# Performance work log

Measured on AMD Instinct MI355X. Metric: run time of the kernel, lower is better.

The kernel has to match this reference:

```python
import jax, jax.numpy as jnp
import numpy as np

B, S, H, NH = 2, 2048, 1024, 16
HD = H // NH  # 64
BASE = 10000.0


def _rope_tables(seq_len, head_dim):
    inv_freq = 1.0 / (BASE ** (jnp.arange(0, head_dim, 2, dtype=jnp.float32) / head_dim))
    t = jnp.arange(seq_len, dtype=jnp.float32)
    freqs = jnp.outer(t, inv_freq)            # [S, HD/2]
    emb = jnp.concatenate([freqs, freqs], -1)  # [S, HD]
    return jnp.cos(emb), jnp.sin(emb)


def _rotate_half(x):
    x1, x2 = jnp.split(x, 2, axis=-1)
    return jnp.concatenate([-x2, x1], axis=-1)


def setup_inputs() -> dict:
    key = jax.random.key(0)
    ks = jax.random.split(key, 5)
    sc = 1.0 / np.sqrt(H)
    return {
        "hidden_states": jax.random.normal(ks[0], (B, S, H), jnp.float32),
        "Wq": jax.random.normal(ks[1], (H, H), jnp.float32) * sc,
        "Wk": jax.random.normal(ks[2], (H, H), jnp.float32) * sc,
        "Wv": jax.random.normal(ks[3], (H, H), jnp.float32) * sc,
        "Wo": jax.random.normal(ks[4], (H, H), jnp.float32) * sc,
    }


def reference(hidden_states, Wq, Wk, Wv, Wo):
    b, s, h = hidden_states.shape
    # nn.Linear: y = x @ W.T
    q = hidden_states @ Wq.T
    k = hidden_states @ Wk.T
    v = hidden_states @ Wv.T
    # [B, NH, S, HD]
    q = q.reshape(b, s, NH, HD).transpose(0, 2, 1, 3)
    k = k.reshape(b, s, NH, HD).transpose(0, 2, 1, 3)
    v = v.reshape(b, s, NH, HD).transpose(0, 2, 1, 3)
    cos, sin = _rope_tables(s, HD)  # [S, HD], broadcast over B, NH
    q = q * cos + _rotate_half(q) * sin
    k = k * cos + _rotate_half(k) * sin
    scores = jnp.einsum('bhqd,bhkd->bhqk', q, k) / jnp.sqrt(jnp.float32(HD))
    probs = jax.nn.softmax(scores, axis=-1)
    ctx = jnp.einsum('bhqk,bhkd->bhqd', probs, v)
    ctx = ctx.transpose(0, 2, 1, 3).reshape(b, s, h)
    return ctx @ Wo.T
```

## Files before the change

### kernel.cpp

```cpp
#include <hip/hip_runtime.h>
#include <hip/hip_bf16.h>
#include <math.h>

typedef __hip_bfloat16 bf16;
typedef float f32x4 __attribute__((ext_vector_type(4)));
typedef float f32x16 __attribute__((ext_vector_type(16)));
typedef short s16x8 __attribute__((ext_vector_type(8)));

#define NB 2
#define SEQ 2048
#define HID 1024
#define NHEAD 16
#define HD 64
#define BH (NB * NHEAD)
#define MROWS (NB * SEQ)
#define QSCL 0.18033688011111793f

static __device__ __forceinline__ f32x4 mfma16(s16x8 a, s16x8 b, f32x4 c) {
  return __builtin_amdgcn_mfma_f32_16x16x32_bf16(a, b, c, 0, 0, 0);
}
static __device__ __forceinline__ f32x16 mfma32(s16x8 a, s16x8 b, f32x16 c) {
  return __builtin_amdgcn_mfma_f32_32x32x16_bf16(a, b, c, 0, 0, 0);
}

static __device__ __forceinline__ void gload_lds16(const bf16* g, bf16* l) {
  __builtin_amdgcn_global_load_lds((const __attribute__((address_space(1))) void*)g,
                                   (__attribute__((address_space(3))) void*)l, 16, 0, 0);
}

static __device__ __forceinline__ unsigned pack_bf16(float a, float b) {
  __hip_bfloat162 t = __float22bfloat162_rn(float2{a, b});
  return *(unsigned*)&t;
}

__global__ __launch_bounds__(256) void prep_kernel(const float* __restrict__ X,
                                                   const float* __restrict__ wq, const float* __restrict__ wk,
                                                   const float* __restrict__ wv, const float* __restrict__ wo,
                                                   bf16* __restrict__ Xb, bf16* __restrict__ wqkv,
                                                   bf16* __restrict__ wob,
                                                   float* __restrict__ ct, float* __restrict__ st) {
  int bid = blockIdx.x, tid = threadIdx.x;
  if (bid < 8192) {
    const float* src;
    bf16* dst;
    int i;
    if (bid < 4096) {
      src = X; dst = Xb;
      i = (bid * 256 + tid) * 4;
    } else {
      int wsel = (bid - 4096) >> 10;
      src = (wsel == 0) ? wq : (wsel == 1) ? wk : (wsel == 2) ? wv : wo;
      dst = (wsel < 3) ? (wqkv + (size_t)wsel * HID * HID) : wob;
      i = (((bid - 4096) & 1023) * 256 + tid) * 4;
    }
    float4 v = *(const float4*)(src + i);
    bf16 a0 = __float2bfloat16(v.x), a1 = __float2bfloat16(v.y);
    bf16 a2 = __float2bfloat16(v.z), a3 = __float2bfloat16(v.w);
    ushort4 u;
    u.x = *(const unsigned short*)&a0;
    u.y = *(const unsigned short*)&a1;
    u.z = *(const unsigned short*)&a2;
    u.w = *(const unsigned short*)&a3;
    *(ushort4*)(dst + i) = u;
  } else {
    int i = (bid - 8192) * 256 + tid;
    int s = i >> 5, j = i & 31;
    float inv = expf(-(float)(2 * j) * (9.210340371976184f / 64.0f));
    float ang = (float)s * inv;
    float sn, cs;
    sincosf(ang, &sn, &cs);
    ct[i] = cs;
    st[i] = sn;
  }
}

template <int MODE>
__global__ __launch_bounds__(256) void gemm_bt(const bf16* __restrict__ A, const bf16* __restrict__ Bm,
                                               float* __restrict__ C,
                                               bf16* __restrict__ Qb, bf16* __restrict__ Kb,
                                               bf16* __restrict__ Vtg,
                                               const float* __restrict__ ct, const float* __restrict__ st,
                                               int M, int N, int K) {
  __shared__ __align__(16) bf16 As[128][32];
  __shared__ __align__(16) bf16 Bs[128][32];
  const int tid = threadIdx.x, lane = tid & 63, wid = tid >> 6;
  const int wm = wid >> 1, wn = wid & 1;
  const int tm = blockIdx.y * 128, tn = blockIdx.x * 128;
  const int lrow = lane >> 2;
  const int lcol = (lane & 3) * 8;

  f32x4 acc[4][4];
#pragma unroll
  for (int i = 0; i < 4; ++i)
#pragma unroll
    for (int j = 0; j < 4; ++j) acc[i][j] = (f32x4){0.f, 0.f, 0.f, 0.f};

  for (int k0 = 0; k0 < K; k0 += 32) {
    __syncthreads();
    {
      int r0 = wid * 32;
      gload_lds16(A  + (size_t)(tm + r0 +      lrow) * K + k0 + lcol, &As[r0][0]);
      gload_lds16(A  + (size_t)(tm + r0 + 16 + lrow) * K + k0 + lcol, &As[r0 + 16][0]);
      gload_lds16(Bm + (size_t)(tn + r0 +      lrow) * K + k0 + lcol, &Bs[r0][0]);
      gload_lds16(Bm + (size_t)(tn + r0 + 16 + lrow) * K + k0 + lcol, &Bs[r0 + 16][0]);
    }
    __syncthreads();
    s16x8 af[4], bfr[4];
#pragma unroll
    for (int mi = 0; mi < 4; ++mi)
      af[mi] = *(const s16x8*)&As[wm * 64 + mi * 16 + (lane & 15)][(lane >> 4) * 8];
#pragma unroll
    for (int ni = 0; ni < 4; ++ni)
      bfr[ni] = *(const s16x8*)&Bs[wn * 64 + ni * 16 + (lane & 15)][(lane >> 4) * 8];
#pragma unroll
    for (int mi = 0; mi < 4; ++mi)
#pragma unroll
      for (int ni = 0; ni < 4; ++ni)
        acc[mi][ni] = mfma16(af[mi], bfr[ni], acc[mi][ni]);
  }

  if (MODE == 0) {
    const int tblk = tn >> 10;
    if (tblk < 2) {
      const float scl = (tblk == 0) ? QSCL : 1.0f;
#pragma unroll
      for (int mi = 0; mi < 4; ++mi) {
#pragma unroll
        for (int r = 0; r < 4; ++r) {
          int row = tm + wm * 64 + mi * 16 + (lane >> 4) * 4 + r;
          int s = row & (SEQ - 1);
#pragma unroll
          for (int p = 0; p < 2; ++p) {
            int j = p * 16 + (lane & 15);
            float c = ct[s * 32 + j], sn = st[s * 32 + j];
            float x0 = acc[mi][p][r], x1 = acc[mi][p + 2][r];
            acc[mi][p][r]     = (x0 * c - x1 * sn) * scl;
            acc[mi][p + 2][r] = (x1 * c + x0 * sn) * scl;
          }
        }
      }
    }
  }

#pragma unroll
  for (int mi = 0; mi < 4; ++mi) {
#pragma unroll
    for (int ni = 0; ni < 4; ++ni) {
#pragma unroll
      for (int r = 0; r < 4; ++r) {
        int row = tm + wm * 64 + mi * 16 + (lane >> 4) * 4 + r;
        int col = tn + wn * 64 + ni * 16 + (lane & 15);
        float v = acc[mi][ni][r];
        if (MODE == 0) {
          int t = col >> 10, c = col & (HID - 1);
          int h = c >> 6, d = c & 63;
          int b = row >> 11, s = row & (SEQ - 1);
          size_t bh = (size_t)(b * NHEAD + h);
          if (t == 0)      Qb[(bh * SEQ + s) * HD + d]  = __float2bfloat16(v);
          else if (t == 1) Kb[(bh * SEQ + s) * HD + d]  = __float2bfloat16(v);
          else             Vtg[(bh * HD + d) * SEQ + s] = __float2bfloat16(v);
        } else {
          C[(size_t)row * N + col] = v;
        }
      }
    }
  }
}

__global__ __launch_bounds__(256) void attn_kernel(const bf16* __restrict__ Q, const bf16* __restrict__ K,
                                                   const bf16* __restrict__ Vt, bf16* __restrict__ ctx) {
  __shared__ __align__(16) bf16 S[16384];
  bf16* Ks = S;
  bf16* Vs = S + 8192;
  const int tid = threadIdx.x, l = tid & 63, w = tid >> 6;
  const int lq = l & 31, hi = l >> 5;

  const int id = blockIdx.x;
  const int lin = (id & 7) * 64 + (id >> 3);
  const int bh = lin >> 4, qb = lin & 15;

  const bf16* Qp  = Q  + ((size_t)bh * SEQ + qb * 128) * HD;
  const bf16* Kp0 = K  + (size_t)bh * SEQ * HD;
  const bf16* Vp0 = Vt + (size_t)bh * HD * SEQ;

  s16x8 qf[4];
  {
    const bf16* qr = Qp + (w * 32 + lq) * HD + hi * 8;
#pragma unroll
    for (int ks = 0; ks < 4; ++ks) qf[ks] = *(const s16x8*)(qr + ks * 16);
  }

  const int s0 = tid, s1 = tid + 256;
  const int R0 = s0 >> 3, R1 = s1 >> 3;
  const int c0 = ((s0 & 7) ^ (R0 & 7)) * 8;
  const int c1 = ((s1 & 7) ^ (R1 & 7)) * 8;
  const int p0 = (R0 & 51) | ((R0 & 4) << 1) | ((R0 & 8) >> 1);
  const int p1 = (R1 & 51) | ((R1 & 4) << 1) | ((R1 & 8) >> 1);
  const bf16* kS0 = Kp0 + p0 * HD + c0;
  const bf16* kS1 = Kp0 + p1 * HD + c1;
  const bf16* vS0 = Vp0 + (size_t)R0 * SEQ + c0;
  const bf16* vS1 = Vp0 + (size_t)R1 * SEQ + c1;

#define STAGE(t, b)                                        \
  do {                                                     \
    gload_lds16(kS0 + (t) * (64 * HD), Ks + (b) * 4096 + s0 * 8); \
    gload_lds16(kS1 + (t) * (64 * HD), Ks + (b) * 4096 + s1 * 8); \
    gload_lds16(vS0 + (t) * 64,        Vs + (b) * 4096 + s0 * 8); \
    gload_lds16(vS1 + (t) * 64,        Vs + (b) * 4096 + s1 * 8); \
  } while (0)

  STAGE(0, 0);
  __syncthreads();

  float m_run = -INFINITY, lsum = 0.f;
  f32x16 acc0{}, acc1{};

  const int NT = SEQ / 64;
  for (int kvt = 0; kvt < NT; ++kvt) {
    const int cur = kvt & 1;
    if (kvt + 1 < NT) STAGE(kvt + 1, cur ^ 1);
    const bf16* Kc = Ks + cur * 4096;
    const bf16* Vc = Vs + cur * 4096;

    f32x16 sf0{}, sf1{};
    __builtin_amdgcn_s_setprio(1);
#pragma unroll
    for (int ks = 0; ks < 4; ++ks) {
      const int slot = (ks * 2 + hi) ^ (lq & 7);
      sf0 = mfma32(*(const s16x8*)(Kc + lq * 64 + slot * 8),        qf[ks], sf0);
      sf1 = mfma32(*(const s16x8*)(Kc + (32 + lq) * 64 + slot * 8), qf[ks], sf1);
    }
    __builtin_amdgcn_s_setprio(0);

    float pmax = sf0[0];
#pragma unroll
    for (int i = 1; i < 16; ++i) pmax = fmaxf(pmax, sf0[i]);
#pragma unroll
    for (int i = 0; i < 16; ++i) pmax = fmaxf(pmax, sf1[i]);
    pmax = fmaxf(pmax, __shfl_xor(pmax, 32));

    if (__any(pmax > m_run + 8.f)) {
      float mn = fmaxf(m_run, pmax);
      float corr = __builtin_amdgcn_exp2f(m_run - mn);
      m_run = mn;
      lsum *= corr;
#pragma unroll
      for (int r = 0; r < 16; ++r) {
        float cr = __shfl(corr, (r & 3) + 8 * (r >> 2) + 4 * hi);
        acc0[r] *= cr;
        acc1[r] *= cr;
      }
    }

    float ls = 0.f;
#pragma unroll
    for (int i = 0; i < 16; ++i) {
      sf0[i] = __builtin_amdgcn_exp2f(sf0[i] - m_run);
      ls += sf0[i];
    }
#pragma unroll
    for (int i = 0; i < 16; ++i) {
      sf1[i] = __builtin_amdgcn_exp2f(sf1[i] - m_run);
      ls += sf1[i];
    }
    lsum += ls;

    s16x8 pf[4];
#pragma unroll
    for (int kt = 0; kt < 4; ++kt) {
      union { unsigned u[4]; s16x8 v; } cc;
#pragma unroll
      for (int vv = 0; vv < 4; ++vv) {
        if (kt < 2) cc.u[vv] = pack_bf16(sf0[(kt & 1) * 8 + 2 * vv], sf0[(kt & 1) * 8 + 2 * vv + 1]);
        else        cc.u[vv] = pack_bf16(sf1[(kt & 1) * 8 + 2 * vv], sf1[(kt & 1) * 8 + 2 * vv + 1]);
      }
      pf[kt] = cc.v;
    }

    __builtin_amdgcn_s_setprio(1);
#pragma unroll
    for (int kt = 0; kt < 4; ++kt) {
      const int slot = (kt * 2 + hi) ^ (lq & 7);
      acc0 = mfma32(pf[kt], *(const s16x8*)(Vc + lq * 64 + slot * 8),        acc0);
      acc1 = mfma32(pf[kt], *(const s16x8*)(Vc + (32 + lq) * 64 + slot * 8), acc1);
    }
    __builtin_amdgcn_s_setprio(0);
    __syncthreads();
  }
#undef STAGE

  lsum += __shfl_xor(lsum, 32);
  const int b = bh >> 4, h = bh & (NHEAD - 1);
#pragma unroll
  for (int r = 0; r < 16; ++r) {
    int q = (r & 3) + 8 * (r >> 2) + 4 * hi;
    float inv = 1.0f / __shfl(lsum, q);
    size_t base = ((size_t)b * SEQ + qb * 128 + w * 32 + q) * HID + h * HD + lq;
    ctx[base]      = __float2bfloat16(acc0[r] * inv);
    ctx[base + 32] = __float2bfloat16(acc1[r] * inv);
  }
}

extern "C" void kernel_launch(void* const* d_in, const int* in_sizes, int n_in,
                              void* d_out, int out_size, void* d_ws, size_t ws_size,
                              hipStream_t stream) {
  const float* X  = (const float*)d_in[0];
  const float* Wq = (const float*)d_in[1];
  const float* Wk = (const float*)d_in[2];
  const float* Wv = (const float*)d_in[3];
  const float* Wo = (const float*)d_in[4];

  char* p = (char*)d_ws;
  bf16* Xb   = (bf16*)p; p += (size_t)MROWS * HID * 2;
  bf16* Wqkv = (bf16*)p; p += (size_t)3 * HID * HID * 2;
  bf16* Wob  = (bf16*)p; p += (size_t)HID * HID * 2;
  bf16* Qb   = (bf16*)p; p += (size_t)BH * SEQ * HD * 2;
  bf16* Kb   = (bf16*)p; p += (size_t)BH * SEQ * HD * 2;
  bf16* Vtg  = (bf16*)p; p += (size_t)BH * HD * SEQ * 2;
  bf16* Cb   = (bf16*)p; p += (size_t)MROWS * HID * 2;
  float* ct  = (float*)p; p += (size_t)SEQ * 32 * 4;
  float* st  = (float*)p; p += (size_t)SEQ * 32 * 4;

  prep_kernel<<<8448, 256, 0, stream>>>(X, Wq, Wk, Wv, Wo, Xb, Wqkv, Wob, ct, st);

  gemm_bt<0><<<dim3(3 * HID / 128, MROWS / 128), 256, 0, stream>>>(
      Xb, Wqkv, nullptr, Qb, Kb, Vtg, ct, st, MROWS, 3 * HID, HID);

  attn_kernel<<<dim3(512), 256, 0, stream>>>(Qb, Kb, Vtg, Cb);

  gemm_bt<1><<<dim3(HID / 128, MROWS / 128), 256, 0, stream>>>(
      Cb, Wob, (float*)d_out, nullptr, nullptr, nullptr, nullptr, nullptr, MROWS, HID, HID);
}
```

Before: 140.7 us.

## Split attention KV range across two wave groups and merge partial softmax results

The attention kernel now runs 512 threads per block as two groups of four waves. Each group processes half of the KV sequence for the same 128 query rows, with its own double-buffered LDS staging. The partial outputs, running maxima and sums are merged through shared memory at the end. This doubles the waves available to hide latency and halves the serial loop length per block, at the cost of doubled LDS use (64KB per block), an extra merge pass, and lower block-level occupancy.

```diff
diff --git a/kernel.cpp b/kernel.cpp
--- a/kernel.cpp
+++ b/kernel.cpp
@@ -167,13 +167,13 @@
   }
 }
 
-__global__ __launch_bounds__(256) void attn_kernel(const bf16* __restrict__ Q, const bf16* __restrict__ K,
-                                                   const bf16* __restrict__ Vt, bf16* __restrict__ ctx) {
-  __shared__ __align__(16) bf16 S[16384];
-  bf16* Ks = S;
-  bf16* Vs = S + 8192;
+__global__ __launch_bounds__(512, 4) void attn_kernel(const bf16* __restrict__ Q, const bf16* __restrict__ K,
+                                                      const bf16* __restrict__ Vt, bf16* __restrict__ ctx) {
+  __shared__ __align__(16) bf16 S[32768];
   const int tid = threadIdx.x, l = tid & 63, w = tid >> 6;
   const int lq = l & 31, hi = l >> 5;
+  const int grp = w >> 2, wq = w & 3;
+  const int gtid = tid & 255;
 
   const int id = blockIdx.x;
   const int lin = (id & 7) * 64 + (id >> 3);
@@ -183,14 +183,17 @@
   const bf16* Kp0 = K  + (size_t)bh * SEQ * HD;
   const bf16* Vp0 = Vt + (size_t)bh * HD * SEQ;
 
+  bf16* Ksg = S + grp * 16384;
+  bf16* Vsg = S + grp * 16384 + 8192;
+
   s16x8 qf[4];
   {
-    const bf16* qr = Qp + (w * 32 + lq) * HD + hi * 8;
+    const bf16* qr = Qp + (wq * 32 + lq) * HD + hi * 8;
 #pragma unroll
     for (int ks = 0; ks < 4; ++ks) qf[ks] = *(const s16x8*)(qr + ks * 16);
   }
 
-  const int s0 = tid, s1 = tid + 256;
+  const int s0 = gtid, s1 = gtid + 256;
   const int R0 = s0 >> 3, R1 = s1 >> 3;
   const int c0 = ((s0 & 7) ^ (R0 & 7)) * 8;
   const int c1 = ((s1 & 7) ^ (R1 & 7)) * 8;
@@ -201,26 +204,26 @@
   const bf16* vS0 = Vp0 + (size_t)R0 * SEQ + c0;
   const bf16* vS1 = Vp0 + (size_t)R1 * SEQ + c1;
 
-#define STAGE(t, b)                                        \
-  do {                                                     \
-    gload_lds16(kS0 + (t) * (64 * HD), Ks + (b) * 4096 + s0 * 8); \
-    gload_lds16(kS1 + (t) * (64 * HD), Ks + (b) * 4096 + s1 * 8); \
-    gload_lds16(vS0 + (t) * 64,        Vs + (b) * 4096 + s0 * 8); \
-    gload_lds16(vS1 + (t) * 64,        Vs + (b) * 4096 + s1 * 8); \
+#define STAGE(t, b)                                                 \
+  do {                                                              \
+    gload_lds16(kS0 + (size_t)(t) * (64 * HD), Ksg + (b) * 4096 + s0 * 8); \
+    gload_lds16(kS1 + (size_t)(t) * (64 * HD), Ksg + (b) * 4096 + s1 * 8); \
+    gload_lds16(vS0 + (t) * 64,                Vsg + (b) * 4096 + s0 * 8); \
+    gload_lds16(vS1 + (t) * 64,                Vsg + (b) * 4096 + s1 * 8); \
   } while (0)
 
-  STAGE(0, 0);
+  STAGE(grp * 16, 0);
   __syncthreads();
 
   float m_run = -INFINITY, lsum = 0.f;
   f32x16 acc0{}, acc1{};
 
-  const int NT = SEQ / 64;
-  for (int kvt = 0; kvt < NT; ++kvt) {
-    const int cur = kvt & 1;
-    if (kvt + 1 < NT) STAGE(kvt + 1, cur ^ 1);
-    const bf16* Kc = Ks + cur * 4096;
-    const bf16* Vc = Vs + cur * 4096;
+  const int NSTEP = 16;
+  for (int i = 0; i < NSTEP; ++i) {
+    const int cur = i & 1;
+    if (i + 1 < NSTEP) STAGE(grp * 16 + i + 1, cur ^ 1);
+    const bf16* Kc = Ksg + cur * 4096;
+    const bf16* Vc = Vsg + cur * 4096;
 
     f32x16 sf0{}, sf1{};
     __builtin_amdgcn_s_setprio(1);
@@ -234,9 +237,9 @@
 
     float pmax = sf0[0];
 #pragma unroll
-    for (int i = 1; i < 16; ++i) pmax = fmaxf(pmax, sf0[i]);
-#pragma unroll
-    for (int i = 0; i < 16; ++i) pmax = fmaxf(pmax, sf1[i]);
+    for (int i2 = 1; i2 < 16; ++i2) pmax = fmaxf(pmax, sf0[i2]);
+#pragma unroll
+    for (int i2 = 0; i2 < 16; ++i2) pmax = fmaxf(pmax, sf1[i2]);
     pmax = fmaxf(pmax, __shfl_xor(pmax, 32));
 
     if (__any(pmax > m_run + 8.f)) {
@@ -254,14 +257,14 @@
 
     float ls = 0.f;
 #pragma unroll
-    for (int i = 0; i < 16; ++i) {
-      sf0[i] = __builtin_amdgcn_exp2f(sf0[i] - m_run);
-      ls += sf0[i];
-    }
-#pragma unroll
-    for (int i = 0; i < 16; ++i) {
-      sf1[i] = __builtin_amdgcn_exp2f(sf1[i] - m_run);
-      ls += sf1[i];
+    for (int i2 = 0; i2 < 16; ++i2) {
+      sf0[i2] = __builtin_amdgcn_exp2f(sf0[i2] - m_run);
+      ls += sf0[i2];
+    }
+#pragma unroll
+    for (int i2 = 0; i2 < 16; ++i2) {
+      sf1[i2] = __builtin_amdgcn_exp2f(sf1[i2] - m_run);
+      ls += sf1[i2];
     }
     lsum += ls;
 
@@ -290,14 +293,45 @@
 #undef STAGE
 
   lsum += __shfl_xor(lsum, 32);
-  const int b = bh >> 4, h = bh & (NHEAD - 1);
-#pragma unroll
-  for (int r = 0; r < 16; ++r) {
-    int q = (r & 3) + 8 * (r >> 2) + 4 * hi;
-    float inv = 1.0f / __shfl(lsum, q);
-    size_t base = ((size_t)b * SEQ + qb * 128 + w * 32 + q) * HID + h * HD + lq;
-    ctx[base]      = __float2bfloat16(acc0[r] * inv);
-    ctx[base + 32] = __float2bfloat16(acc1[r] * inv);
+
+  float* Op = (float*)(S + 16384);
+  float* Mp = (float*)(S);
+  float* Lp = Mp + 128;
+
+  if (grp == 1) {
+    if (hi == 0) {
+      Mp[wq * 32 + lq] = m_run;
+      Lp[wq * 32 + lq] = lsum;
+    }
+#pragma unroll
+    for (int r = 0; r < 16; ++r) {
+      int q = (r & 3) + 8 * (r >> 2) + 4 * hi;
+      Op[(wq * 32 + q) * 64 + lq]      = acc0[r];
+      Op[(wq * 32 + q) * 64 + 32 + lq] = acc1[r];
+    }
+  }
+  __syncthreads();
+
+  if (grp == 0) {
+    float m1 = Mp[wq * 32 + lq], l1 = Lp[wq * 32 + lq];
+    float mN = fmaxf(m_run, m1);
+    float cr0 = __builtin_amdgcn_exp2f(m_run - mN);
+    float cr1 = __builtin_amdgcn_exp2f(m1 - mN);
+    float inv = 1.0f / (lsum * cr0 + l1 * cr1);
+
+    const int b = bh >> 4, h = bh & (NHEAD - 1);
+#pragma unroll
+    for (int r = 0; r < 16; ++r) {
+      int q = (r & 3) + 8 * (r >> 2) + 4 * hi;
+      float c0q = __shfl(cr0, q);
+      float c1q = __shfl(cr1, q);
+      float invq = __shfl(inv, q);
+      float o0 = (acc0[r] * c0q + Op[(wq * 32 + q) * 64 + lq]      * c1q) * invq;
+      float o1 = (acc1[r] * c0q + Op[(wq * 32 + q) * 64 + 32 + lq] * c1q) * invq;
+      size_t base = ((size_t)b * SEQ + qb * 128 + wq * 32 + q) * HID + h * HD + lq;
+      ctx[base]      = __float2bfloat16(o0);
+      ctx[base + 32] = __float2bfloat16(o1);
+    }
   }
 }
 
@@ -326,7 +360,7 @@
   gemm_bt<0><<<dim3(3 * HID / 128, MROWS / 128), 256, 0, stream>>>(
       Xb, Wqkv, nullptr, Qb, Kb, Vtg, ct, st, MROWS, 3 * HID, HID);
 
-  attn_kernel<<<dim3(512), 256, 0, stream>>>(Qb, Kb, Vtg, Cb);
+  attn_kernel<<<dim3(512), 512, 0, stream>>>(Qb, Kb, Vtg, Cb);
 
   gemm_bt<1><<<dim3(HID / 128, MROWS / 128), 256, 0, stream>>>(
       Cb, Wob, (float*)d_out, nullptr, nullptr, nullptr, nullptr, nullptr, MROWS, HID, HID);
```

Result: no change. 138.0 us (-1.9%).
